# Kernel optimization log

Measured on AMD Instinct MI355X. Metric: run time of the kernel, lower is better.

Reference implementation:

```python
import jax, jax.numpy as jnp
import numpy as np

B, T, C, HEAD = 4, 4096, 2048, 128
ROPE_BASE = 10000.0


def _rope_tables(T, dim):
    # precompute_freqs_cis: freqs = 1/base^(2i/dim), angles = t * freqs
    inv_freq = 1.0 / (ROPE_BASE ** (np.arange(0, dim, 2, dtype=np.float32) / dim))
    angles = np.arange(T, dtype=np.float32)[:, None] * inv_freq[None, :]  # [T, dim/2]
    return jnp.asarray(np.cos(angles)), jnp.asarray(np.sin(angles))


def _apply_rope(x, cos, sin):
    # x: [B, T, D]; interleaved complex pairs (x[2i], x[2i+1]) rotated by angle
    B_, T_, D = x.shape
    xr = x.reshape(B_, T_, D // 2, 2)
    x1, x2 = xr[..., 0], xr[..., 1]
    o1 = x1 * cos - x2 * sin
    o2 = x1 * sin + x2 * cos
    return jnp.stack([o1, o2], axis=-1).reshape(B_, T_, D)


def setup_inputs() -> dict:
    key0 = jax.random.key(0)
    k1, k2, k3, k4 = jax.random.split(key0, 4)
    x = jax.random.normal(k1, (B, T, C), dtype=jnp.float32)
    key = jax.random.normal(k2, (B, T, HEAD), dtype=jnp.float32)
    value = jax.random.normal(k3, (B, T, HEAD), dtype=jnp.float32)
    w_q = jax.random.normal(k4, (HEAD, C), dtype=jnp.float32) * 0.02
    return {"x": x, "key": key, "value": value, "w_q": w_q}


def reference(x, key, value, w_q):
    # query projection (nn.Linear, no bias)
    q = jnp.einsum('btc,dc->btd', x, w_q)  # [B, T, HEAD]
    cos, sin = _rope_tables(T, HEAD)
    # apply_rotary_emb(key, query) returns (key_rot, query_rot); then
    # query, key = (key_rot, query_rot) and wei = key @ query^T == q_rot @ k_rot^T
    q_rot = _apply_rope(q, cos, sin)
    k_rot = _apply_rope(key, cos, sin)
    scale = HEAD ** -0.5
    wei = jnp.einsum('btd,bsd->bts', q_rot, k_rot) * scale  # [B, T, T]
    causal = jnp.tril(jnp.ones((T, T), dtype=bool))
    wei = jnp.where(causal, wei, -jnp.inf)
    wei = jax.nn.softmax(wei, axis=-1)
    # dropout is identity in eval / p=0
    return jnp.einsum('bts,bsd->btd', wei, value)  # [B, T, HEAD]
```

## Files before the change

### kernel.cpp

```cpp
#include <hip/hip_runtime.h>
#include <hip/hip_bf16.h>

#define TSEQ  4096
#define NBATCH 4
#define CDIM  2048
#define DH    128

typedef __bf16 bf16x8 __attribute__((ext_vector_type(8)));
typedef float  f32x4  __attribute__((ext_vector_type(4)));
typedef unsigned short u16x8 __attribute__((ext_vector_type(8)));
typedef unsigned       u32x4 __attribute__((ext_vector_type(4)));
typedef unsigned short u16;

__device__ __forceinline__ u16 f2bf(float f) {
  union { float f; unsigned u; } v; v.f = f;
  unsigned r = (v.u + 0x7FFFu + ((v.u >> 16) & 1u)) >> 16;
  return (u16)r;
}

__device__ __forceinline__ float bf2f(u16 h) {
  union { unsigned u; float f; } v; v.u = ((unsigned)h) << 16;
  return v.f;
}

__device__ __forceinline__ bf16x8 ld_bf8(const u16* p) {
  return __builtin_bit_cast(bf16x8, *(const u16x8*)p);
}

__device__ __forceinline__ unsigned pk2(float lo, float hi) {
  float2 f; f.x = lo; f.y = hi;
  __hip_bfloat162 h = __float22bfloat162_rn(f);
  unsigned r;
  __builtin_memcpy(&r, &h, 4);
  return r;
}
__device__ __forceinline__ bf16x8 cvt8(float4 a, float4 b) {
  u32x4 u;
  u[0] = pk2(a.x, a.y); u[1] = pk2(a.z, a.w);
  u[2] = pk2(b.x, b.y); u[3] = pk2(b.z, b.w);
  return __builtin_bit_cast(bf16x8, u);
}

template<int CTRL>
__device__ __forceinline__ float dppmv(float x) {
  return __builtin_bit_cast(float,
    __builtin_amdgcn_update_dpp(0, __builtin_bit_cast(int, x), CTRL, 0xF, 0xF, true));
}
__device__ __forceinline__ float red_max16(float v) {
  v = fmaxf(v, dppmv<0xB1>(v));
  v = fmaxf(v, dppmv<0x4E>(v));
  v = fmaxf(v, dppmv<0x124>(v));
  v = fmaxf(v, dppmv<0x128>(v));
  return v;
}
__device__ __forceinline__ float red_sum16(float v) {
  v += dppmv<0xB1>(v);
  v += dppmv<0x4E>(v);
  v += dppmv<0x124>(v);
  v += dppmv<0x128>(v);
  return v;
}

__global__ void k_trig(float* __restrict__ ct, float* __restrict__ st) {
  int i = blockIdx.x * 256 + threadIdx.x;
  int p = i & 63;
  int t = i >> 6;
  float inv = powf(10000.0f, -(float)p / 64.0f);
  float ang = (float)t * inv;
  float s, c; sincosf(ang, &s, &c);
  ct[i] = c; st[i] = s;
}

__global__ void k_wconv(const float* __restrict__ w, u16* __restrict__ wbf) {
  int i = blockIdx.x * 256 + threadIdx.x;
  const float4 v = *(const float4*)(w + (size_t)i * 4);
  uint2 o; o.x = pk2(v.x, v.y); o.y = pk2(v.z, v.w);
  *(uint2*)(wbf + (size_t)i * 4) = o;
}

__global__ void k_ropek(const float* __restrict__ key, const float* __restrict__ ct,
                        const float* __restrict__ st, u16* __restrict__ krot) {
  int g = blockIdx.x * 256 + threadIdx.x;
  int p = g & 63;
  int row = g >> 6;
  int t = row & (TSEQ - 1);
  const float2 kv = *(const float2*)(key + (size_t)row * DH + 2 * p);
  float c = ct[t * 64 + p];
  float s = st[t * 64 + p];
  float o1 = kv.x * c - kv.y * s;
  float o2 = kv.x * s + kv.y * c;
  *(unsigned*)(krot + (size_t)row * DH + 2 * p) = pk2(o1, o2);
}

__global__ void k_vt(const float* __restrict__ v, u16* __restrict__ vt) {
  __shared__ u16 S[128 * 66];
  int bid = blockIdx.x;
  int b = bid >> 6;
  int t0 = (bid & 63) * 64;
  int tid = threadIdx.x;
  int d = (tid & 31) * 4;
  int tl0 = tid >> 5;
#pragma unroll
  for (int i = 0; i < 8; ++i) {
    int tl = tl0 + i * 8;
    const float4 val = *(const float4*)(v + ((size_t)(b * TSEQ + t0 + tl)) * DH + d);
    S[(d + 0) * 66 + tl] = f2bf(val.x);
    S[(d + 1) * 66 + tl] = f2bf(val.y);
    S[(d + 2) * 66 + tl] = f2bf(val.z);
    S[(d + 3) * 66 + tl] = f2bf(val.w);
  }
  __syncthreads();
#pragma unroll
  for (int i = 0; i < 16; ++i) {
    int idx = tid + i * 256;
    int dd = idx >> 5;
    int tw = (idx & 31) * 2;
    unsigned lo = S[dd * 66 + tw];
    unsigned hi = S[dd * 66 + tw + 1];
    *(unsigned*)(vt + ((size_t)(b * DH + dd)) * TSEQ + t0 + tw) = lo | (hi << 16);
  }
}

__global__ __launch_bounds__(256, 2) void k_qproj(const float* __restrict__ x,
                                                  const u16* __restrict__ wbf,
                                                  const float* __restrict__ ct,
                                                  const float* __restrict__ st,
                                                  u16* __restrict__ qrot) {
  __shared__ float Al[32 * 68];
  int bid = blockIdx.x;
  int tid = threadIdx.x;
  int w = tid >> 6;
  int lane = tid & 63;
  int l15 = lane & 15;
  int quad = lane >> 4;
  int m0 = bid * 32;

  int srow = tid >> 3;
  int sc8 = (tid & 7) * 8;
  const float* xg = x + (size_t)(m0 + srow) * CDIM + sc8;

  f32x4 acc[2][2];
#pragma unroll
  for (int mt = 0; mt < 2; ++mt)
#pragma unroll
    for (int nt = 0; nt < 2; ++nt) acc[mt][nt] = (f32x4){0.f, 0.f, 0.f, 0.f};

  float4 pa0 = *(const float4*)(xg);
  float4 pa1 = *(const float4*)(xg + 4);

  for (int it = 0; it < CDIM / 64; ++it) {
    __syncthreads();
    *(float4*)&Al[srow * 68 + sc8] = pa0;
    *(float4*)&Al[srow * 68 + sc8 + 4] = pa1;
    __syncthreads();
    if (it + 1 < CDIM / 64) {
      const float* xn = xg + (size_t)(it + 1) * 64;
      pa0 = *(const float4*)(xn);
      pa1 = *(const float4*)(xn + 4);
    }
    int k0 = it * 64;
#pragma unroll
    for (int ks = 0; ks < 2; ++ks) {
      bf16x8 af[2];
#pragma unroll
      for (int mt = 0; mt < 2; ++mt) {
        const float* ap = &Al[(mt * 16 + l15) * 68 + ks * 32 + quad * 8];
        float4 f0 = *(const float4*)(ap);
        float4 f1 = *(const float4*)(ap + 4);
        af[mt] = cvt8(f0, f1);
      }
#pragma unroll
      for (int nt = 0; nt < 2; ++nt) {
        bf16x8 bfrag = ld_bf8(wbf + (size_t)(w * 32 + nt * 16 + l15) * CDIM + k0 + ks * 32 + quad * 8);
#pragma unroll
        for (int mt = 0; mt < 2; ++mt)
          acc[mt][nt] = __builtin_amdgcn_mfma_f32_16x16x32_bf16(af[mt], bfrag, acc[mt][nt], 0, 0, 0);
      }
    }
  }

  const float scale = 0.08838834764831845f;
#pragma unroll
  for (int mt = 0; mt < 2; ++mt)
#pragma unroll
    for (int nt = 0; nt < 2; ++nt) {
      int dcol = w * 32 + nt * 16 + l15;
      int p = dcol >> 1;
#pragma unroll
      for (int r = 0; r < 4; ++r) {
        int m = m0 + mt * 16 + quad * 4 + r;
        int t = m & (TSEQ - 1);
        float val = acc[mt][nt][r];
        float partner = __shfl_xor(val, 1, 64);
        float c = ct[t * 64 + p];
        float s = st[t * 64 + p];
        float o = (lane & 1) ? (val * c + partner * s) : (val * c - partner * s);
        qrot[(size_t)m * DH + dcol] = f2bf(o * scale);
      }
    }
}

__global__ __launch_bounds__(256) void k_attn(const u16* __restrict__ qrot,
                                              const u16* __restrict__ krot,
                                              const u16* __restrict__ vt,
                                              u16* __restrict__ Opart,
                                              float2* __restrict__ ml) {
  __shared__ u16 Kl[16 * 64 * 8];
  __shared__ u16 Vl[8 * 128 * 8];
  __shared__ u16 Pl[4 * 16 * 72];

  int bid = blockIdx.x;
  int b = bid / 160;
  int u = bid - b * 160;
  int qt, kc;
  if (u < 16)      { qt = u;                kc = 0; }
  else if (u < 48) { qt = 16 + ((u - 16) >> 1); kc = (u - 16) & 1; }
  else if (u < 96) { int q3 = (u - 48) / 3; qt = 32 + q3; kc = (u - 48) - 3 * q3; }
  else             { qt = 48 + ((u - 96) >> 2); kc = (u - 96) & 3; }
  int kt0 = kc * 16;
  int kt1 = min(kt0 + 16, qt + 1);

  int tid = threadIdx.x;
  int w = tid >> 6;
  int lane = tid & 63;
  int l15 = lane & 15;
  int quad = lane >> 4;
  u16* pw = Pl + w * 16 * 72;

  int rK  = tid & 63;   int jgK = tid >> 6;
  int dV  = tid & 127;  int hV  = tid >> 7;

  const u16* kb = krot + (size_t)b * TSEQ * DH;
  const u16* vb = vt + (size_t)b * DH * TSEQ;

  bf16x8 qf[4];
  {
    const u16* qb = qrot + ((size_t)(b * TSEQ + qt * 64 + w * 16 + l15)) * DH + quad * 8;
#pragma unroll
    for (int c = 0; c < 4; ++c) qf[c] = ld_bf8(qb + c * 32);
  }

  f32x4 o_acc[8];
#pragma unroll
  for (int i = 0; i < 8; ++i) o_acc[i] = (f32x4){0.f, 0.f, 0.f, 0.f};
  float m_st[4], l_st[4];
#pragma unroll
  for (int r = 0; r < 4; ++r) { m_st[r] = -INFINITY; l_st[r] = 0.f; }

  u16x8 kr[4], vr[4];
  {
    const u16* ks = kb + (size_t)(kt0 * 64 + rK) * DH + jgK * 32;
    const u16* vs = vb + (size_t)dV * TSEQ + kt0 * 64 + hV * 32;
#pragma unroll
    for (int i = 0; i < 4; ++i) { kr[i] = *(const u16x8*)(ks + i * 8); vr[i] = *(const u16x8*)(vs + i * 8); }
  }

  for (int kt = kt0; kt < kt1; ++kt) {
    __syncthreads();
#pragma unroll
    for (int i = 0; i < 4; ++i) {
      *(u16x8*)&Kl[((jgK * 4 + i) * 64 + rK) * 8] = kr[i];
      *(u16x8*)&Vl[((hV * 4 + i) * 128 + dV) * 8] = vr[i];
    }
    __syncthreads();
    if (kt + 1 < kt1) {
      const u16* ks = kb + (size_t)((kt + 1) * 64 + rK) * DH + jgK * 32;
      const u16* vs = vb + (size_t)dV * TSEQ + (kt + 1) * 64 + hV * 32;
#pragma unroll
      for (int i = 0; i < 4; ++i) { kr[i] = *(const u16x8*)(ks + i * 8); vr[i] = *(const u16x8*)(vs + i * 8); }
    }

    f32x4 s[4];
#pragma unroll
    for (int nt = 0; nt < 4; ++nt) {
      s[nt] = (f32x4){0.f, 0.f, 0.f, 0.f};
#pragma unroll
      for (int c = 0; c < 4; ++c) {
        bf16x8 kf = ld_bf8(&Kl[((c * 4 + quad) * 64 + nt * 16 + l15) * 8]);
        s[nt] = __builtin_amdgcn_mfma_f32_16x16x32_bf16(qf[c], kf, s[nt], 0, 0, 0);
      }
    }
    if (kt == qt) {
#pragma unroll
      for (int nt = 0; nt < 4; ++nt)
#pragma unroll
        for (int r = 0; r < 4; ++r) {
          if (nt * 16 + l15 > w * 16 + quad * 4 + r) s[nt][r] = -INFINITY;
        }
    }
    float alpha[4];
#pragma unroll
    for (int r = 0; r < 4; ++r) {
      float rm = fmaxf(fmaxf(s[0][r], s[1][r]), fmaxf(s[2][r], s[3][r]));
      rm = red_max16(rm);
      float mn = fmaxf(m_st[r], rm);
      float al = __expf(m_st[r] - mn);
      m_st[r] = mn;
      float ps = 0.f;
#pragma unroll
      for (int nt = 0; nt < 4; ++nt) {
        float pv = __expf(s[nt][r] - mn);
        s[nt][r] = pv;
        ps += pv;
      }
      ps = red_sum16(ps);
      l_st[r] = l_st[r] * al + ps;
      alpha[r] = al;
    }
#pragma unroll
    for (int nt = 0; nt < 8; ++nt)
#pragma unroll
      for (int r = 0; r < 4; ++r) o_acc[nt][r] *= alpha[r];
#pragma unroll
    for (int nt = 0; nt < 4; ++nt)
#pragma unroll
      for (int r = 0; r < 4; ++r)
        pw[(quad * 4 + r) * 72 + nt * 16 + l15] = f2bf(s[nt][r]);
#pragma unroll
    for (int c2 = 0; c2 < 2; ++c2) {
      bf16x8 pf = ld_bf8(pw + l15 * 72 + c2 * 32 + quad * 8);
#pragma unroll
      for (int nt = 0; nt < 8; ++nt) {
        bf16x8 vf = ld_bf8(&Vl[((c2 * 4 + quad) * 128 + nt * 16 + l15) * 8]);
        o_acc[nt] = __builtin_amdgcn_mfma_f32_16x16x32_bf16(pf, vf, o_acc[nt], 0, 0, 0);
      }
    }
  }

  int slot = bid;
  u16* op = Opart + (size_t)slot * 8192;
#pragma unroll
  for (int nt = 0; nt < 8; ++nt)
#pragma unroll
    for (int r = 0; r < 4; ++r)
      op[(w * 16 + quad * 4 + r) * 128 + nt * 16 + l15] = f2bf(o_acc[nt][r]);
  if (l15 == 0) {
#pragma unroll
    for (int r = 0; r < 4; ++r) {
      float2 p; p.x = m_st[r]; p.y = l_st[r];
      ml[slot * 64 + w * 16 + quad * 4 + r] = p;
    }
  }
}

__global__ __launch_bounds__(256) void k_merge(const u16* __restrict__ Opart,
                                               const float2* __restrict__ ml,
                                               float* __restrict__ out) {
  __shared__ float wgt[4][64];
  __shared__ float invL[64];
  int bid = blockIdx.x;
  int b = bid >> 6, qt = bid & 63;
  int C = 1 + (qt >> 4);
  int base = b * 160 + (qt < 16 ? qt
                       : qt < 32 ? 16 + 2 * (qt - 16)
                       : qt < 48 ? 48 + 3 * (qt - 32)
                       : 96 + 4 * (qt - 48));
  int tid = threadIdx.x;
  if (tid < 64) {
    float mv[4], lv[4];
    float M = -INFINITY;
    for (int uu = 0; uu < C; ++uu) {
      float2 p = ml[(base + uu) * 64 + tid];
      mv[uu] = p.x; lv[uu] = p.y;
      M = fmaxf(M, p.x);
    }
    float L = 0.f;
    for (int uu = 0; uu < C; ++uu) {
      float wv = __expf(mv[uu] - M);
      wgt[uu][tid] = wv;
      L += wv * lv[uu];
    }
    invL[tid] = 1.f / L;
  }
  __syncthreads();
#pragma unroll
  for (int k = 0; k < 32; ++k) {
    int e = tid + k * 256;
    int row = e >> 7;
    float acc = 0.f;
    for (int uu = 0; uu < C; ++uu)
      acc += wgt[uu][row] * bf2f(Opart[(size_t)(base + uu) * 8192 + e]);
    out[(size_t)(b * TSEQ + qt * 64) * DH + e] = acc * invL[row];
  }
}

extern "C" void kernel_launch(void* const* d_in, const int* in_sizes, int n_in,
                              void* d_out, int out_size, void* d_ws, size_t ws_size,
                              hipStream_t stream) {
  const float* x     = (const float*)d_in[0];
  const float* key   = (const float*)d_in[1];
  const float* value = (const float*)d_in[2];
  const float* w_q   = (const float*)d_in[3];
  float* out = (float*)d_out;

  char* ws = (char*)d_ws;
  u16* wbf    = (u16*)(ws);
  u16* qrot   = (u16*)(ws + (512u << 10));
  u16* krot   = (u16*)(ws + (512u << 10) + (4u << 20));
  u16* vt     = (u16*)(ws + (512u << 10) + (8u << 20));
  float* ct   = (float*)(ws + (512u << 10) + (12u << 20));
  float* st   = (float*)(ws + (512u << 10) + (13u << 20));
  u16* Opart  = (u16*)(ws + (512u << 10) + (14u << 20));
  float2* ml  = (float2*)(ws + (512u << 10) + (24u << 20));

  k_trig<<<(TSEQ * 64) / 256, 256, 0, stream>>>(ct, st);
  k_wconv<<<256, 256, 0, stream>>>(w_q, wbf);
  k_ropek<<<(NBATCH * TSEQ * 64) / 256, 256, 0, stream>>>(key, ct, st, krot);
  k_vt<<<NBATCH * (TSEQ / 64), 256, 0, stream>>>(value, vt);
  k_qproj<<<(NBATCH * TSEQ) / 32, 256, 0, stream>>>(x, wbf, ct, st, qrot);
  k_attn<<<NBATCH * 160, 256, 0, stream>>>(qrot, krot, vt, Opart, ml);
  k_merge<<<NBATCH * 64, 256, 0, stream>>>(Opart, ml, out);
}
```

Measured before the change: 340.0 us.

## Use 128-row query tiles in attention, fuse prep kernels, vectorize merge

The attention kernel now processes 128 query rows per block as two 64-row subtiles, so each K/V tile staged in LDS feeds twice as many MFMAs. Key splits are 8 tiles per unit, scheduled with a closed-form unit_base mapping. The kernel skips the o_acc rescale when no running max changed, and adds a 2-waves occupancy hint. The four preprocessing kernels are fused into one launch, with key RoPE computing sin/cos inline. The merge now reads with 8-wide vector loads and writes float4. This adds register pressure from the doubled accumulators and fewer, coarser blocks.

```diff
diff --git a/kernel.cpp b/kernel.cpp
--- a/kernel.cpp
+++ b/kernel.cpp
@@ -17,21 +17,17 @@
   unsigned r = (v.u + 0x7FFFu + ((v.u >> 16) & 1u)) >> 16;
   return (u16)r;
 }
-
 __device__ __forceinline__ float bf2f(u16 h) {
   union { unsigned u; float f; } v; v.u = ((unsigned)h) << 16;
   return v.f;
 }
-
 __device__ __forceinline__ bf16x8 ld_bf8(const u16* p) {
   return __builtin_bit_cast(bf16x8, *(const u16x8*)p);
 }
-
 __device__ __forceinline__ unsigned pk2(float lo, float hi) {
   float2 f; f.x = lo; f.y = hi;
   __hip_bfloat162 h = __float22bfloat162_rn(f);
-  unsigned r;
-  __builtin_memcpy(&r, &h, 4);
+  unsigned r; __builtin_memcpy(&r, &h, 4);
   return r;
 }
 __device__ __forceinline__ bf16x8 cvt8(float4 a, float4 b) {
@@ -61,63 +57,66 @@
   return v;
 }
 
-__global__ void k_trig(float* __restrict__ ct, float* __restrict__ st) {
-  int i = blockIdx.x * 256 + threadIdx.x;
-  int p = i & 63;
-  int t = i >> 6;
-  float inv = powf(10000.0f, -(float)p / 64.0f);
-  float ang = (float)t * inv;
-  float s, c; sincosf(ang, &s, &c);
-  ct[i] = c; st[i] = s;
-}
-
-__global__ void k_wconv(const float* __restrict__ w, u16* __restrict__ wbf) {
-  int i = blockIdx.x * 256 + threadIdx.x;
-  const float4 v = *(const float4*)(w + (size_t)i * 4);
-  uint2 o; o.x = pk2(v.x, v.y); o.y = pk2(v.z, v.w);
-  *(uint2*)(wbf + (size_t)i * 4) = o;
-}
-
-__global__ void k_ropek(const float* __restrict__ key, const float* __restrict__ ct,
-                        const float* __restrict__ st, u16* __restrict__ krot) {
-  int g = blockIdx.x * 256 + threadIdx.x;
-  int p = g & 63;
-  int row = g >> 6;
-  int t = row & (TSEQ - 1);
-  const float2 kv = *(const float2*)(key + (size_t)row * DH + 2 * p);
-  float c = ct[t * 64 + p];
-  float s = st[t * 64 + p];
-  float o1 = kv.x * c - kv.y * s;
-  float o2 = kv.x * s + kv.y * c;
-  *(unsigned*)(krot + (size_t)row * DH + 2 * p) = pk2(o1, o2);
-}
-
-__global__ void k_vt(const float* __restrict__ v, u16* __restrict__ vt) {
+__device__ __forceinline__ int unit_base(int Q) {
+  int a = Q >> 2, bq = Q & 3;
+  return 2 * a * (a + 1) + bq * (a + 1);
+}
+
+__global__ __launch_bounds__(256) void k_prep(const float* __restrict__ w, u16* __restrict__ wbf,
+                                              const float* __restrict__ key, u16* __restrict__ krot,
+                                              const float* __restrict__ value, u16* __restrict__ vt,
+                                              float* __restrict__ ct, float* __restrict__ st) {
   __shared__ u16 S[128 * 66];
   int bid = blockIdx.x;
-  int b = bid >> 6;
-  int t0 = (bid & 63) * 64;
   int tid = threadIdx.x;
-  int d = (tid & 31) * 4;
-  int tl0 = tid >> 5;
-#pragma unroll
-  for (int i = 0; i < 8; ++i) {
-    int tl = tl0 + i * 8;
-    const float4 val = *(const float4*)(v + ((size_t)(b * TSEQ + t0 + tl)) * DH + d);
-    S[(d + 0) * 66 + tl] = f2bf(val.x);
-    S[(d + 1) * 66 + tl] = f2bf(val.y);
-    S[(d + 2) * 66 + tl] = f2bf(val.z);
-    S[(d + 3) * 66 + tl] = f2bf(val.w);
-  }
-  __syncthreads();
-#pragma unroll
-  for (int i = 0; i < 16; ++i) {
-    int idx = tid + i * 256;
-    int dd = idx >> 5;
-    int tw = (idx & 31) * 2;
-    unsigned lo = S[dd * 66 + tw];
-    unsigned hi = S[dd * 66 + tw + 1];
-    *(unsigned*)(vt + ((size_t)(b * DH + dd)) * TSEQ + t0 + tw) = lo | (hi << 16);
+  if (bid < 256) {
+    int i = bid * 256 + tid;
+    const float4 v = *(const float4*)(w + (size_t)i * 4);
+    uint2 o; o.x = pk2(v.x, v.y); o.y = pk2(v.z, v.w);
+    *(uint2*)(wbf + (size_t)i * 4) = o;
+  } else if (bid < 1280) {
+    int i = (bid - 256) * 256 + tid;
+    int p = i & 63;
+    int t = i >> 6;
+    float inv = powf(10000.0f, -(float)p / 64.0f);
+    float ang = (float)t * inv;
+    float s, c; sincosf(ang, &s, &c);
+    ct[i] = c; st[i] = s;
+  } else if (bid < 5376) {
+    int g = (bid - 1280) * 256 + tid;
+    int p = g & 63;
+    int row = g >> 6;
+    int t = row & (TSEQ - 1);
+    const float2 kv = *(const float2*)(key + (size_t)row * DH + 2 * p);
+    float inv = powf(10000.0f, -(float)p / 64.0f);
+    float ang = (float)t * inv;
+    float s, c; sincosf(ang, &s, &c);
+    *(unsigned*)(krot + (size_t)row * DH + 2 * p) = pk2(kv.x * c - kv.y * s, kv.x * s + kv.y * c);
+  } else {
+    int vb = bid - 5376;
+    int b = vb >> 6;
+    int t0 = (vb & 63) * 64;
+    int d = (tid & 31) * 4;
+    int tl0 = tid >> 5;
+#pragma unroll
+    for (int i = 0; i < 8; ++i) {
+      int tl = tl0 + i * 8;
+      const float4 val = *(const float4*)(value + ((size_t)(b * TSEQ + t0 + tl)) * DH + d);
+      S[(d + 0) * 66 + tl] = f2bf(val.x);
+      S[(d + 1) * 66 + tl] = f2bf(val.y);
+      S[(d + 2) * 66 + tl] = f2bf(val.z);
+      S[(d + 3) * 66 + tl] = f2bf(val.w);
+    }
+    __syncthreads();
+#pragma unroll
+    for (int i = 0; i < 16; ++i) {
+      int idx = tid + i * 256;
+      int dd = idx >> 5;
+      int tw = (idx & 31) * 2;
+      unsigned lo = S[dd * 66 + tw];
+      unsigned hi = S[dd * 66 + tw + 1];
+      *(unsigned*)(vt + ((size_t)(b * DH + dd)) * TSEQ + t0 + tw) = lo | (hi << 16);
+    }
   }
 }
 
@@ -200,52 +199,60 @@
     }
 }
 
-__global__ __launch_bounds__(256) void k_attn(const u16* __restrict__ qrot,
-                                              const u16* __restrict__ krot,
-                                              const u16* __restrict__ vt,
-                                              u16* __restrict__ Opart,
-                                              float2* __restrict__ ml) {
+__global__ __launch_bounds__(256, 2) void k_attn(const u16* __restrict__ qrot,
+                                                 const u16* __restrict__ krot,
+                                                 const u16* __restrict__ vt,
+                                                 u16* __restrict__ Opart,
+                                                 float2* __restrict__ ml) {
   __shared__ u16 Kl[16 * 64 * 8];
   __shared__ u16 Vl[8 * 128 * 8];
-  __shared__ u16 Pl[4 * 16 * 72];
+  __shared__ u16 Pl[4 * 32 * 72];
 
   int bid = blockIdx.x;
-  int b = bid / 160;
-  int u = bid - b * 160;
-  int qt, kc;
-  if (u < 16)      { qt = u;                kc = 0; }
-  else if (u < 48) { qt = 16 + ((u - 16) >> 1); kc = (u - 16) & 1; }
-  else if (u < 96) { int q3 = (u - 48) / 3; qt = 32 + q3; kc = (u - 48) - 3 * q3; }
-  else             { qt = 48 + ((u - 96) >> 2); kc = (u - 96) & 3; }
-  int kt0 = kc * 16;
-  int kt1 = min(kt0 + 16, qt + 1);
+  int b = bid / 144;
+  int u = bid - b * 144;
+  int Q = 0;
+#pragma unroll 1
+  for (int q = 31; q >= 0; --q) {
+    if (unit_base(q) <= u) { Q = q; break; }
+  }
+  int kc = u - unit_base(Q);
+  int nkt = 2 * Q + 2;
+  int kt0 = kc * 8;
+  int kt1 = min(kt0 + 8, nkt);
+  int m0 = Q * 128;
 
   int tid = threadIdx.x;
   int w = tid >> 6;
   int lane = tid & 63;
   int l15 = lane & 15;
   int quad = lane >> 4;
-  u16* pw = Pl + w * 16 * 72;
-
-  int rK  = tid & 63;   int jgK = tid >> 6;
-  int dV  = tid & 127;  int hV  = tid >> 7;
+  u16* pw = Pl + w * 32 * 72;
+
+  int rK = tid & 63;   int jgK = tid >> 6;
+  int dV = tid & 127;  int hV = tid >> 7;
 
   const u16* kb = krot + (size_t)b * TSEQ * DH;
   const u16* vb = vt + (size_t)b * DH * TSEQ;
 
-  bf16x8 qf[4];
-  {
-    const u16* qb = qrot + ((size_t)(b * TSEQ + qt * 64 + w * 16 + l15)) * DH + quad * 8;
-#pragma unroll
-    for (int c = 0; c < 4; ++c) qf[c] = ld_bf8(qb + c * 32);
-  }
-
-  f32x4 o_acc[8];
-#pragma unroll
-  for (int i = 0; i < 8; ++i) o_acc[i] = (f32x4){0.f, 0.f, 0.f, 0.f};
-  float m_st[4], l_st[4];
-#pragma unroll
-  for (int r = 0; r < 4; ++r) { m_st[r] = -INFINITY; l_st[r] = 0.f; }
+  bf16x8 qf[2][4];
+#pragma unroll
+  for (int mt = 0; mt < 2; ++mt) {
+    const u16* qb = qrot + ((size_t)(b * TSEQ + m0 + mt * 64 + w * 16 + l15)) * DH + quad * 8;
+#pragma unroll
+    for (int c = 0; c < 4; ++c) qf[mt][c] = ld_bf8(qb + c * 32);
+  }
+
+  f32x4 o_acc[2][8];
+#pragma unroll
+  for (int mt = 0; mt < 2; ++mt)
+#pragma unroll
+    for (int i = 0; i < 8; ++i) o_acc[mt][i] = (f32x4){0.f, 0.f, 0.f, 0.f};
+  float m_st[2][4], l_st[2][4];
+#pragma unroll
+  for (int mt = 0; mt < 2; ++mt)
+#pragma unroll
+    for (int r = 0; r < 4; ++r) { m_st[mt][r] = -INFINITY; l_st[mt][r] = 0.f; }
 
   u16x8 kr[4], vr[4];
   {
@@ -270,117 +277,156 @@
       for (int i = 0; i < 4; ++i) { kr[i] = *(const u16x8*)(ks + i * 8); vr[i] = *(const u16x8*)(vs + i * 8); }
     }
 
-    f32x4 s[4];
-#pragma unroll
-    for (int nt = 0; nt < 4; ++nt) {
-      s[nt] = (f32x4){0.f, 0.f, 0.f, 0.f};
-#pragma unroll
-      for (int c = 0; c < 4; ++c) {
+    f32x4 s[2][4];
+#pragma unroll
+    for (int mt = 0; mt < 2; ++mt)
+#pragma unroll
+      for (int nt = 0; nt < 4; ++nt) s[mt][nt] = (f32x4){0.f, 0.f, 0.f, 0.f};
+#pragma unroll
+    for (int c = 0; c < 4; ++c)
+#pragma unroll
+      for (int nt = 0; nt < 4; ++nt) {
         bf16x8 kf = ld_bf8(&Kl[((c * 4 + quad) * 64 + nt * 16 + l15) * 8]);
-        s[nt] = __builtin_amdgcn_mfma_f32_16x16x32_bf16(qf[c], kf, s[nt], 0, 0, 0);
-      }
-    }
-    if (kt == qt) {
+#pragma unroll
+        for (int mt = 0; mt < 2; ++mt)
+          s[mt][nt] = __builtin_amdgcn_mfma_f32_16x16x32_bf16(qf[mt][c], kf, s[mt][nt], 0, 0, 0);
+      }
+
+    if (kt * 64 >= m0) {
+#pragma unroll
+      for (int mt = 0; mt < 2; ++mt)
+#pragma unroll
+        for (int nt = 0; nt < 4; ++nt)
+#pragma unroll
+          for (int r = 0; r < 4; ++r) {
+            int key_g = kt * 64 + nt * 16 + l15;
+            int row_g = m0 + mt * 64 + w * 16 + quad * 4 + r;
+            if (key_g > row_g) s[mt][nt][r] = -INFINITY;
+          }
+    }
+
+    float alpha[2][4];
+    int chg = 0;
+#pragma unroll
+    for (int mt = 0; mt < 2; ++mt)
+#pragma unroll
+      for (int r = 0; r < 4; ++r) {
+        float rm = fmaxf(fmaxf(s[mt][0][r], s[mt][1][r]), fmaxf(s[mt][2][r], s[mt][3][r]));
+        rm = red_max16(rm);
+        float mn = fmaxf(m_st[mt][r], rm);
+        float al = __expf(m_st[mt][r] - mn);
+        m_st[mt][r] = mn;
+        float ps = 0.f;
+#pragma unroll
+        for (int nt = 0; nt < 4; ++nt) {
+          float pv = __expf(s[mt][nt][r] - mn);
+          s[mt][nt][r] = pv;
+          ps += pv;
+        }
+        ps = red_sum16(ps);
+        l_st[mt][r] = l_st[mt][r] * al + ps;
+        alpha[mt][r] = al;
+        chg |= (al != 1.0f);
+      }
+    if (__any(chg)) {
+#pragma unroll
+      for (int mt = 0; mt < 2; ++mt)
+#pragma unroll
+        for (int nt = 0; nt < 8; ++nt)
+#pragma unroll
+          for (int r = 0; r < 4; ++r) o_acc[mt][nt][r] *= alpha[mt][r];
+    }
+
+#pragma unroll
+    for (int mt = 0; mt < 2; ++mt)
 #pragma unroll
       for (int nt = 0; nt < 4; ++nt)
 #pragma unroll
-        for (int r = 0; r < 4; ++r) {
-          if (nt * 16 + l15 > w * 16 + quad * 4 + r) s[nt][r] = -INFINITY;
-        }
-    }
-    float alpha[4];
-#pragma unroll
-    for (int r = 0; r < 4; ++r) {
-      float rm = fmaxf(fmaxf(s[0][r], s[1][r]), fmaxf(s[2][r], s[3][r]));
-      rm = red_max16(rm);
-      float mn = fmaxf(m_st[r], rm);
-      float al = __expf(m_st[r] - mn);
-      m_st[r] = mn;
-      float ps = 0.f;
-#pragma unroll
-      for (int nt = 0; nt < 4; ++nt) {
-        float pv = __expf(s[nt][r] - mn);
-        s[nt][r] = pv;
-        ps += pv;
-      }
-      ps = red_sum16(ps);
-      l_st[r] = l_st[r] * al + ps;
-      alpha[r] = al;
-    }
-#pragma unroll
-    for (int nt = 0; nt < 8; ++nt)
-#pragma unroll
-      for (int r = 0; r < 4; ++r) o_acc[nt][r] *= alpha[r];
-#pragma unroll
-    for (int nt = 0; nt < 4; ++nt)
-#pragma unroll
-      for (int r = 0; r < 4; ++r)
-        pw[(quad * 4 + r) * 72 + nt * 16 + l15] = f2bf(s[nt][r]);
+        for (int r = 0; r < 4; ++r)
+          pw[(mt * 16 + quad * 4 + r) * 72 + nt * 16 + l15] = f2bf(s[mt][nt][r]);
+
 #pragma unroll
     for (int c2 = 0; c2 < 2; ++c2) {
-      bf16x8 pf = ld_bf8(pw + l15 * 72 + c2 * 32 + quad * 8);
+      bf16x8 pf[2];
+#pragma unroll
+      for (int mt = 0; mt < 2; ++mt)
+        pf[mt] = ld_bf8(pw + (mt * 16 + l15) * 72 + c2 * 32 + quad * 8);
 #pragma unroll
       for (int nt = 0; nt < 8; ++nt) {
         bf16x8 vf = ld_bf8(&Vl[((c2 * 4 + quad) * 128 + nt * 16 + l15) * 8]);
-        o_acc[nt] = __builtin_amdgcn_mfma_f32_16x16x32_bf16(pf, vf, o_acc[nt], 0, 0, 0);
-      }
-    }
-  }
-
-  int slot = bid;
-  u16* op = Opart + (size_t)slot * 8192;
-#pragma unroll
-  for (int nt = 0; nt < 8; ++nt)
-#pragma unroll
-    for (int r = 0; r < 4; ++r)
-      op[(w * 16 + quad * 4 + r) * 128 + nt * 16 + l15] = f2bf(o_acc[nt][r]);
+#pragma unroll
+        for (int mt = 0; mt < 2; ++mt)
+          o_acc[mt][nt] = __builtin_amdgcn_mfma_f32_16x16x32_bf16(pf[mt], vf, o_acc[mt][nt], 0, 0, 0);
+      }
+    }
+  }
+
+  u16* op = Opart + (size_t)bid * (128 * 128);
+#pragma unroll
+  for (int mt = 0; mt < 2; ++mt)
+#pragma unroll
+    for (int nt = 0; nt < 8; ++nt)
+#pragma unroll
+      for (int r = 0; r < 4; ++r)
+        op[(mt * 64 + w * 16 + quad * 4 + r) * 128 + nt * 16 + l15] = f2bf(o_acc[mt][nt][r]);
   if (l15 == 0) {
 #pragma unroll
-    for (int r = 0; r < 4; ++r) {
-      float2 p; p.x = m_st[r]; p.y = l_st[r];
-      ml[slot * 64 + w * 16 + quad * 4 + r] = p;
-    }
+    for (int mt = 0; mt < 2; ++mt)
+#pragma unroll
+      for (int r = 0; r < 4; ++r) {
+        float2 p; p.x = m_st[mt][r]; p.y = l_st[mt][r];
+        ml[(size_t)bid * 128 + mt * 64 + w * 16 + quad * 4 + r] = p;
+      }
   }
 }
 
 __global__ __launch_bounds__(256) void k_merge(const u16* __restrict__ Opart,
                                                const float2* __restrict__ ml,
                                                float* __restrict__ out) {
-  __shared__ float wgt[4][64];
-  __shared__ float invL[64];
+  __shared__ float wgt[8][128];
+  __shared__ float invL[128];
   int bid = blockIdx.x;
-  int b = bid >> 6, qt = bid & 63;
-  int C = 1 + (qt >> 4);
-  int base = b * 160 + (qt < 16 ? qt
-                       : qt < 32 ? 16 + 2 * (qt - 16)
-                       : qt < 48 ? 48 + 3 * (qt - 32)
-                       : 96 + 4 * (qt - 48));
+  int b = bid >> 5, Q = bid & 31;
+  int C = (Q >> 2) + 1;
+  int base = b * 144 + unit_base(Q);
   int tid = threadIdx.x;
-  if (tid < 64) {
-    float mv[4], lv[4];
+  if (tid < 128) {
+    float mv[8], lv[8];
     float M = -INFINITY;
-    for (int uu = 0; uu < C; ++uu) {
-      float2 p = ml[(base + uu) * 64 + tid];
-      mv[uu] = p.x; lv[uu] = p.y;
+    for (int c = 0; c < C; ++c) {
+      float2 p = ml[(size_t)(base + c) * 128 + tid];
+      mv[c] = p.x; lv[c] = p.y;
       M = fmaxf(M, p.x);
     }
     float L = 0.f;
-    for (int uu = 0; uu < C; ++uu) {
-      float wv = __expf(mv[uu] - M);
-      wgt[uu][tid] = wv;
-      L += wv * lv[uu];
+    for (int c = 0; c < C; ++c) {
+      float wv = __expf(mv[c] - M);
+      wgt[c][tid] = wv;
+      L += wv * lv[c];
     }
     invL[tid] = 1.f / L;
   }
   __syncthreads();
 #pragma unroll
-  for (int k = 0; k < 32; ++k) {
-    int e = tid + k * 256;
-    int row = e >> 7;
-    float acc = 0.f;
-    for (int uu = 0; uu < C; ++uu)
-      acc += wgt[uu][row] * bf2f(Opart[(size_t)(base + uu) * 8192 + e]);
-    out[(size_t)(b * TSEQ + qt * 64) * DH + e] = acc * invL[row];
+  for (int k = 0; k < 8; ++k) {
+    int slot = tid + k * 256;
+    int row = slot >> 4;
+    float acc[8];
+#pragma unroll
+    for (int j = 0; j < 8; ++j) acc[j] = 0.f;
+    for (int c = 0; c < C; ++c) {
+      u16x8 v = *(const u16x8*)&Opart[(size_t)(base + c) * (128 * 128) + slot * 8];
+      float wv = wgt[c][row];
+#pragma unroll
+      for (int j = 0; j < 8; ++j) acc[j] += wv * bf2f(v[j]);
+    }
+    float il = invL[row];
+    float4 o0, o1;
+    o0.x = acc[0] * il; o0.y = acc[1] * il; o0.z = acc[2] * il; o0.w = acc[3] * il;
+    o1.x = acc[4] * il; o1.y = acc[5] * il; o1.z = acc[6] * il; o1.w = acc[7] * il;
+    float* op = out + ((size_t)(b * TSEQ + Q * 128 + row)) * DH + (slot & 15) * 8;
+    *(float4*)op = o0;
+    *(float4*)(op + 4) = o1;
   }
 }
 
@@ -401,13 +447,10 @@
   float* ct   = (float*)(ws + (512u << 10) + (12u << 20));
   float* st   = (float*)(ws + (512u << 10) + (13u << 20));
   u16* Opart  = (u16*)(ws + (512u << 10) + (14u << 20));
-  float2* ml  = (float2*)(ws + (512u << 10) + (24u << 20));
-
-  k_trig<<<(TSEQ * 64) / 256, 256, 0, stream>>>(ct, st);
-  k_wconv<<<256, 256, 0, stream>>>(w_q, wbf);
-  k_ropek<<<(NBATCH * TSEQ * 64) / 256, 256, 0, stream>>>(key, ct, st, krot);
-  k_vt<<<NBATCH * (TSEQ / 64), 256, 0, stream>>>(value, vt);
+  float2* ml  = (float2*)(ws + (512u << 10) + (34u << 20));
+
+  k_prep<<<5632, 256, 0, stream>>>(w_q, wbf, key, krot, value, vt, ct, st);
   k_qproj<<<(NBATCH * TSEQ) / 32, 256, 0, stream>>>(x, wbf, ct, st, qrot);
-  k_attn<<<NBATCH * 160, 256, 0, stream>>>(qrot, krot, vt, Opart, ml);
-  k_merge<<<NBATCH * 64, 256, 0, stream>>>(Opart, ml, out);
-}
+  k_attn<<<NBATCH * 144, 256, 0, stream>>>(qrot, krot, vt, Opart, ml);
+  k_merge<<<NBATCH * 32, 256, 0, stream>>>(Opart, ml, out);
+}
```

Result: faster. 297.1 us (-12.6%).
